# Optimization experiments

Hardware: AMD Instinct MI355X
Metric: run time of the kernel (lower is better)

Reference implementation:

```python
import jax, jax.numpy as jnp
import numpy as np

N, F, H, R, DEG, K = 8192, 64, 128, 3, 32, 32
TEMP = 0.3          # config.edge_temperature
NEG_SLOPE = 0.2     # LeakyReLU slope
EPS_LN = 1e-5
W_THRESH = 1e-6


def setup_inputs() -> dict:
    key = jax.random.key(0)
    ks = jax.random.split(key, 16)
    E = N * DEG
    # each node has DEG outgoing edges so no softmax row is empty (-inf everywhere)
    src = jnp.repeat(jnp.arange(N), DEG)
    tgt = jax.random.randint(ks[0], (E,), 0, N)
    edge_index = jnp.stack([src, tgt]).astype(jnp.int64)
    x = jax.random.normal(ks[1], (N, F), jnp.float32)
    edge_attr = jax.random.normal(ks[2], (E, 3), jnp.float32)
    s = lambda k, sh: jax.random.normal(k, sh, jnp.float32) * 0.05
    D = 2 * F + 3  # edge_input_dim
    params = dict(
        Ws1=s(ks[3], (D, H)), bs1=jnp.zeros(H), ln_g=jnp.ones(H), ln_b=jnp.zeros(H),
        Ws2=s(ks[4], (H, 1)), bs2=jnp.zeros(1),
        Wp=s(ks[5], (D, H)), bp=jnp.zeros(H),
        Wr1=s(ks[6], (F, H)), br1=jnp.zeros(H), Wr2=s(ks[7], (H, R)), br2=jnp.zeros(R),
        Wg1=s(ks[8], (R, H, H // 2)), bg1=jnp.zeros((R, H // 2)),
        Wg2=s(ks[9], (R, H // 2, 1)), bg2=jnp.zeros((R, 1)),
        Wc1=s(ks[10], (F, H)), bc1=jnp.zeros(H), Wc2=s(ks[11], (H, 1)), bc2=jnp.zeros(1),
    )
    return {"x": x, "edge_index": edge_index, "edge_attr": edge_attr, **params}


def reference(x, edge_index, edge_attr,
              Ws1, bs1, ln_g, ln_b, Ws2, bs2, Wp, bp,
              Wr1, br1, Wr2, br2, Wg1, bg1, Wg2, bg2,
              Wc1, bc1, Wc2, bc2):
    src, tgt = edge_index[0], edge_index[1]
    num_nodes = x.shape[0]

    # regime encoder on global mean state
    gs = x.mean(axis=0)
    regime_probs = jax.nn.softmax(jax.nn.relu(gs @ Wr1 + br1) @ Wr2 + br2)  # [R]

    # contagion detector (scalar level)
    contagion_level = jax.nn.sigmoid(jax.nn.relu(x @ Wc1 + bc1) @ Wc2 + bc2).mean()

    # gather -> edge MLP scorer with LayerNorm + LeakyReLU
    edge_input = jnp.concatenate([x[src], x[tgt], edge_attr], axis=-1)  # [E, 2F+3]
    h = edge_input @ Ws1 + bs1
    mu = h.mean(-1, keepdims=True)
    var = h.var(-1, keepdims=True)
    h = (h - mu) * jax.lax.rsqrt(var + EPS_LN) * ln_g + ln_b
    h = jnp.where(h >= 0, h, NEG_SLOPE * h)
    edge_scores_raw = h @ Ws2 + bs2  # [E, 1]

    # regime gating
    edge_hidden = jax.nn.relu(edge_input @ Wp + bp)  # [E, H]
    g1 = jax.nn.relu(jnp.einsum('eh,rhm->erm', edge_hidden, Wg1) + bg1)
    gates = jax.nn.sigmoid(jnp.einsum('erm,rmo->ero', g1, Wg2) + bg2)[..., 0]  # [E, R]
    gate_combined = (gates * regime_probs).sum(-1, keepdims=True)  # [E, 1]

    amp = 1.0 + 0.5 * contagion_level
    edge_scores = (edge_scores_raw * gate_combined * amp)[:, 0]  # [E]

    # scatter into dense NxN, masked softmax per source row, top-k
    M = jnp.full((num_nodes, num_nodes), -jnp.inf, x.dtype).at[src, tgt].set(edge_scores)
    P = jax.nn.softmax(M / TEMP, axis=-1)  # [N, N]
    topk_values, topk_indices = jax.lax.top_k(P, K)  # [N, K]

    # in-device compaction equivalent: weights below threshold zeroed (dropped edges)
    new_edge_weights = jnp.where(topk_values > W_THRESH, topk_values, 0.0)  # [N, K]
    return new_edge_weights, topk_indices
```

## Files before the change

kernel.cpp:

```cpp
#include <hip/hip_runtime.h>
#include <hip/hip_bf16.h>
#include <math.h>

#define NN 8192
#define FF 64
#define HH 128
#define RR 3
#define DEG 32
#define KK 32
#define EE (NN*DEG)
#define DD 131
#define TEMP 0.3f
#define NEG_SLOPE 0.2f
#define EPS_LN 1e-5f
#define W_THRESH 1e-6f

__device__ __forceinline__ float4 ld4(const float* p) { return *(const float4*)p; }


__global__ __launch_bounds__(256) void stats_kernel(
    const float* __restrict__ x, const float* __restrict__ Wc1,
    const float* __restrict__ bc1, const float* __restrict__ Wc2,
    const float* __restrict__ bc2, float* __restrict__ hdr)
{
    __shared__ float xs[64 * 65];
    __shared__ float wl[64 * 128];
    __shared__ float cs[4][64];
    int t = threadIdx.x;
    int n0 = blockIdx.x * 64;

    for (int i = 0; i < 16; i++) {
        int flat = t + i * 256;
        int r = flat >> 6, c = flat & 63;
        xs[r * 65 + c] = x[(n0 + r) * 64 + c];
    }
    for (int i = 0; i < 32; i++) {
        int flat = t + i * 256;
        wl[flat] = Wc1[flat];
    }
    __syncthreads();

    {
        int col = t & 63, g = t >> 6;
        float ps = 0.f;
        for (int r = g * 16; r < g * 16 + 16; r++) ps += xs[r * 65 + col];
        cs[g][col] = ps;
    }
    __syncthreads();
    if (t < 64) {
        float v = cs[0][t] + cs[1][t] + cs[2][t] + cs[3][t];
        atomicAdd(&hdr[8 + t], v);
    }

    int r = t >> 2, q = t & 3;
    float accl = 0.f;
    for (int hh = 0; hh < 32; hh++) {
        int h = hh * 4 + q;
        float s = bc1[h];
        for (int i = 0; i < 64; i++) s += xs[r * 65 + i] * wl[i * 128 + h];
        accl += fmaxf(s, 0.f) * Wc2[h];
    }
    accl += __shfl_xor(accl, 1);
    accl += __shfl_xor(accl, 2);
    if (q == 0) {
        float lvl = 1.f / (1.f + expf(-(accl + bc2[0])));
        atomicAdd(&hdr[0], lvl);
    }
}

__global__ __launch_bounds__(128) void regime_kernel(
    const float* __restrict__ Wr1, const float* __restrict__ br1,
    const float* __restrict__ Wr2, const float* __restrict__ br2,
    float* __restrict__ hdr)
{
    __shared__ float gsl[64];
    __shared__ float t1[128];
    int t = threadIdx.x;
    if (t < 64) gsl[t] = hdr[8 + t] * (1.f / (float)NN);
    __syncthreads();
    float a = br1[t];
    for (int i = 0; i < 64; i++) a += gsl[i] * Wr1[i * 128 + t];
    t1[t] = fmaxf(a, 0.f);
    __syncthreads();
    if (t < 3) {
        float v = br2[t];
        for (int h = 0; h < 128; h++) v += t1[h] * Wr2[h * 3 + t];
        gsl[32 + t] = v;
    }
    __syncthreads();
    if (t == 0) {
        float v0 = gsl[32], v1 = gsl[33], v2 = gsl[34];
        float m = fmaxf(v0, fmaxf(v1, v2));
        float e0 = expf(v0 - m), e1 = expf(v1 - m), e2 = expf(v2 - m);
        float inv = 1.f / (e0 + e1 + e2);
        hdr[1] = e0 * inv; hdr[2] = e1 * inv; hdr[3] = e2 * inv;
        hdr[4] = 1.f + 0.5f * (hdr[0] * (1.f / (float)NN));
    }
}

__global__ __launch_bounds__(256) void partial_kernel(
    const float* __restrict__ x, const float* __restrict__ Ws1,
    const float* __restrict__ Wp, float* __restrict__ PA)
{
    __shared__ float xs[32 * 65];
    __shared__ float wl[64 * 128];
    int t = threadIdx.x;
    int which = blockIdx.x & 1;
    int n0 = (blockIdx.x >> 1) * 32;
    const float* base = which ? Wp : Ws1;

    for (int i = t; i < 2048; i += 256)
        xs[(i >> 6) * 65 + (i & 63)] = x[n0 * 64 + i];
    for (int it = 0; it < 8; it++) {
        int flat = (t + it * 256) * 4;
        *(float4*)&wl[flat] = ld4(&base[flat]);
    }
    __syncthreads();

    int row = t >> 3, colg = t & 7;
    float acc[16];
    #pragma unroll
    for (int j = 0; j < 16; j++) acc[j] = 0.f;
    const float* xr = &xs[row * 65];
    for (int k = 0; k < 64; k++) {
        float a = xr[k];
        const float* wr = &wl[k * 128 + colg * 16];
        #pragma unroll
        for (int jj = 0; jj < 4; jj++) {
            float4 w = ld4(wr + 4 * jj);
            acc[4*jj+0] += a * w.x; acc[4*jj+1] += a * w.y;
            acc[4*jj+2] += a * w.z; acc[4*jj+3] += a * w.w;
        }
    }
    float* outp = PA + (size_t)which * (NN * 128) + (size_t)(n0 + row) * 128 + colg * 16;
    #pragma unroll
    for (int j = 0; j < 16; j++) outp[j] = acc[j];
}

#define EIB_STRIDE 76
#define EHT_STRIDE 68
__global__ __launch_bounds__(256) void edge_score_kernel(
    const int* __restrict__ tgt_idx, const float* __restrict__ edge_attr,
    const float* __restrict__ x,
    const float* __restrict__ Ws1, const float* __restrict__ bs1,
    const float* __restrict__ ln_g, const float* __restrict__ ln_b,
    const float* __restrict__ Ws2, const float* __restrict__ bs2,
    const float* __restrict__ Wp, const float* __restrict__ bp,
    const float* __restrict__ Wg1, const float* __restrict__ bg1,
    const float* __restrict__ Wg2, const float* __restrict__ bg2,
    const float* __restrict__ PA1, const float* __restrict__ PA2,
    const float* __restrict__ hdr, float* __restrict__ scores)
{
    __shared__ float pool[13184];
    float* EIB   = pool;
    float* WPan  = pool + 4864;
    float* ehT   = pool;
    float* WgG   = pool + 8704;
    float* rawS  = pool + 13056;
    float* gateC = pool + 13120;

    int t = threadIdx.x;
    int e0 = blockIdx.x * 64;

    {
        int r = t >> 2, q = t & 3;
        int ge = e0 + r;
        int tg = tgt_idx[ge];
        for (int ii = q; ii < EIB_STRIDE; ii += 4) {
            float v;
            if (ii < 64) v = x[tg * 64 + ii];
            else if (ii < 67) v = edge_attr[ge * 3 + (ii - 64)];
            else v = 0.f;
            EIB[r * EIB_STRIDE + ii] = v;
        }
    }

    int tcol = t & 7, trow = t >> 3;
    const float* EIr0 = &EIB[(2 * trow) * EIB_STRIDE];
    const float* EIr1 = EIr0 + EIB_STRIDE;
    int src0 = (e0 + 2 * trow) >> 5;
    int src1 = (e0 + 2 * trow + 1) >> 5;

    float accs0[16], accs1[16], accp0[16], accp1[16];

    {
        const float* p1a = &PA1[(size_t)src0 * 128 + tcol * 4];
        const float* p1b = &PA1[(size_t)src1 * 128 + tcol * 4];
        const float* p2a = &PA2[(size_t)src0 * 128 + tcol * 4];
        const float* p2b = &PA2[(size_t)src1 * 128 + tcol * 4];
        #pragma unroll
        for (int jj = 0; jj < 4; jj++) {
            float4 v;
            v = ld4(p1a + jj * 32);
            accs0[4*jj+0]=v.x; accs0[4*jj+1]=v.y; accs0[4*jj+2]=v.z; accs0[4*jj+3]=v.w;
            v = ld4(p1b + jj * 32);
            accs1[4*jj+0]=v.x; accs1[4*jj+1]=v.y; accs1[4*jj+2]=v.z; accs1[4*jj+3]=v.w;
            v = ld4(p2a + jj * 32);
            accp0[4*jj+0]=v.x; accp0[4*jj+1]=v.y; accp0[4*jj+2]=v.z; accp0[4*jj+3]=v.w;
            v = ld4(p2b + jj * 32);
            accp1[4*jj+0]=v.x; accp1[4*jj+1]=v.y; accp1[4*jj+2]=v.z; accp1[4*jj+3]=v.w;
        }
    }

    for (int p = 0; p < 3; p++) {
        __syncthreads();
        #pragma unroll
        for (int i = 0; i < 6; i++) {
            int fid = i * 256 + t;
            int mat = (fid >= 768) ? 1 : 0;
            int loc = fid - mat * 768;
            int pr = loc >> 5;
            int pc = (loc & 31) * 4;
            int wrow = 64 + p * 24 + pr;
            const float* Wsrc = mat ? Wp : Ws1;
            float4 w = (wrow < 131) ? ld4(&Wsrc[wrow * 128 + pc])
                                    : make_float4(0.f, 0.f, 0.f, 0.f);
            *(float4*)&WPan[mat * 3072 + pr * 128 + pc] = w;
        }
        __syncthreads();
        for (int kk = 0; kk < 24; kk++) {
            int k = p * 24 + kk;
            float a0 = EIr0[k];
            float a1 = EIr1[k];
            const float* ws = &WPan[kk * 128 + tcol * 4];
            const float* wq = &WPan[3072 + kk * 128 + tcol * 4];
            #pragma unroll
            for (int jj = 0; jj < 4; jj++) {
                float4 w1 = ld4(ws + jj * 32);
                accs0[jj*4+0] += a0 * w1.x; accs0[jj*4+1] += a0 * w1.y;
                accs0[jj*4+2] += a0 * w1.z; accs0[jj*4+3] += a0 * w1.w;
                accs1[jj*4+0] += a1 * w1.x; accs1[jj*4+1] += a1 * w1.y;
                accs1[jj*4+2] += a1 * w1.z; accs1[jj*4+3] += a1 * w1.w;
                float4 w2 = ld4(wq + jj * 32);
                accp0[jj*4+0] += a0 * w2.x; accp0[jj*4+1] += a0 * w2.y;
                accp0[jj*4+2] += a0 * w2.z; accp0[jj*4+3] += a0 * w2.w;
                accp1[jj*4+0] += a1 * w2.x; accp1[jj*4+1] += a1 * w2.y;
                accp1[jj*4+2] += a1 * w2.z; accp1[jj*4+3] += a1 * w2.w;
            }
        }
    }

    {
        float s0 = 0.f, ss0 = 0.f, s1 = 0.f, ss1 = 0.f;
        #pragma unroll
        for (int j = 0; j < 16; j++) {
            int col = tcol * 4 + (j >> 2) * 32 + (j & 3);
            float b = bs1[col];
            accs0[j] += b; accs1[j] += b;
            s0 += accs0[j]; ss0 += accs0[j] * accs0[j];
            s1 += accs1[j]; ss1 += accs1[j] * accs1[j];
        }
        #pragma unroll
        for (int m = 1; m < 8; m <<= 1) {
            s0 += __shfl_xor(s0, m);  ss0 += __shfl_xor(ss0, m);
            s1 += __shfl_xor(s1, m);  ss1 += __shfl_xor(ss1, m);
        }
        float mu0 = s0 * (1.f / 128.f), mu1 = s1 * (1.f / 128.f);
        float var0 = ss0 * (1.f / 128.f) - mu0 * mu0;
        float var1 = ss1 * (1.f / 128.f) - mu1 * mu1;
        float inv0 = 1.f / sqrtf(var0 + EPS_LN);
        float inv1 = 1.f / sqrtf(var1 + EPS_LN);
        float d0 = 0.f, d1 = 0.f;
        #pragma unroll
        for (int j = 0; j < 16; j++) {
            int col = tcol * 4 + (j >> 2) * 32 + (j & 3);
            float g = ln_g[col], bb = ln_b[col], w2 = Ws2[col];
            float y0 = (accs0[j] - mu0) * inv0 * g + bb;
            float y1 = (accs1[j] - mu1) * inv1 * g + bb;
            y0 = (y0 >= 0.f) ? y0 : NEG_SLOPE * y0;
            y1 = (y1 >= 0.f) ? y1 : NEG_SLOPE * y1;
            d0 += y0 * w2; d1 += y1 * w2;
        }
        #pragma unroll
        for (int m = 1; m < 8; m <<= 1) {
            d0 += __shfl_xor(d0, m); d1 += __shfl_xor(d1, m);
        }
        if (tcol == 0) {
            rawS[2 * trow]     = d0 + bs2[0];
            rawS[2 * trow + 1] = d1 + bs2[0];
        }
    }

    __syncthreads();
    #pragma unroll
    for (int j = 0; j < 16; j++) {
        int col = tcol * 4 + (j >> 2) * 32 + (j & 3);
        float b = bp[col];
        ehT[col * EHT_STRIDE + 2 * trow]     = fmaxf(accp0[j] + b, 0.f);
        ehT[col * EHT_STRIDE + 2 * trow + 1] = fmaxf(accp1[j] + b, 0.f);
    }

    {
        int gtr = t >> 4, gtc = t & 15;
        int grow = t >> 2, gq = t & 3;
        float rp0 = hdr[1], rp1 = hdr[2], rp2 = hdr[3];
        float gc = 0.f;
        for (int rr = 0; rr < 3; rr++) {
            float acc[16];
            #pragma unroll
            for (int j = 0; j < 16; j++) acc[j] = 0.f;
            for (int p = 0; p < 2; p++) {
                __syncthreads();
                #pragma unroll
                for (int i = 0; i < 4; i++) {
                    int fid = i * 256 + t;
                    int pr = fid >> 4;
                    int pc = (fid & 15) * 4;
                    *(float4*)&WgG[pr * 64 + pc] =
                        ld4(&Wg1[(size_t)(rr * 128 + p * 64 + pr) * 64 + pc]);
                }
                __syncthreads();
                for (int kk = 0; kk < 64; kk++) {
                    float4 av = ld4(&ehT[(p * 64 + kk) * EHT_STRIDE + 4 * gtr]);
                    float4 bv = ld4(&WgG[kk * 64 + 4 * gtc]);
                    acc[0]  += av.x * bv.x; acc[1]  += av.x * bv.y; acc[2]  += av.x * bv.z; acc[3]  += av.x * bv.w;
                    acc[4]  += av.y * bv.x; acc[5]  += av.y * bv.y; acc[6]  += av.y * bv.z; acc[7]  += av.y * bv.w;
                    acc[8]  += av.z * bv.x; acc[9]  += av.z * bv.y; acc[10] += av.z * bv.z; acc[11] += av.z * bv.w;
                    acc[12] += av.w * bv.x; acc[13] += av.w * bv.y; acc[14] += av.w * bv.z; acc[15] += av.w * bv.w;
                }
            }
            __syncthreads();
            #pragma unroll
            for (int j = 0; j < 4; j++) {
                float b = bg1[rr * 64 + 4 * gtc + j];
                float4 g;
                g.x = fmaxf(acc[0  + j] + b, 0.f);
                g.y = fmaxf(acc[4  + j] + b, 0.f);
                g.z = fmaxf(acc[8  + j] + b, 0.f);
                g.w = fmaxf(acc[12 + j] + b, 0.f);
                *(float4*)&WgG[(4 * gtc + j) * EHT_STRIDE + 4 * gtr] = g;
            }
            __syncthreads();
            float pacc = 0.f;
            #pragma unroll
            for (int j = 0; j < 16; j++) {
                int m = gq * 4 + (j >> 2) * 16 + (j & 3);
                pacc += WgG[m * EHT_STRIDE + grow] * Wg2[rr * 64 + m];
            }
            pacc += __shfl_xor(pacc, 1);
            pacc += __shfl_xor(pacc, 2);
            float gate = 1.f / (1.f + expf(-(pacc + bg2[rr])));
            float rpr = (rr == 0) ? rp0 : ((rr == 1) ? rp1 : rp2);
            gc += gate * rpr;
        }
        if (gq == 0) gateC[grow] = gc;
    }
    __syncthreads();

    if (t < 64) scores[e0 + t] = rawS[t] * gateC[t] * hdr[4];
}

__global__ __launch_bounds__(64) void finalize_kernel(
    const int* __restrict__ tgt_idx, const float* __restrict__ scores,
    float* __restrict__ out_w, float* __restrict__ out_i)
{
    __shared__ int   tl[32];
    __shared__ float pl[32];
    int j = threadIdx.x;
    int row = blockIdx.x;
    bool lane_active = (j < 32);
    int   tg = 0;
    float s  = -INFINITY;
    if (lane_active) {
        tg = tgt_idx[row * 32 + j];
        s  = scores[row * 32 + j];
        tl[j] = tg;
    }
    __syncthreads();

    bool alive = false;
    if (lane_active) {
        alive = true;
        for (int j2 = j + 1; j2 < 32; j2++)
            if (tl[j2] == tg) { alive = false; break; }
    }
    float z = (lane_active && alive) ? s * (1.f / TEMP) : -INFINITY;
    float m = z;
    #pragma unroll
    for (int mm = 1; mm < 64; mm <<= 1) m = fmaxf(m, __shfl_xor(m, mm));
    float p = (lane_active && alive) ? expf(z - m) : 0.f;
    float sum = p;
    #pragma unroll
    for (int mm = 1; mm < 64; mm <<= 1) sum += __shfl_xor(sum, mm);
    p = p / sum;
    if (lane_active) pl[j] = alive ? p : -1.f;
    __syncthreads();

    int rank = 0, dcount = 0;
    for (int j2 = 0; j2 < 32; j2++) {
        float pj = pl[j2];
        if (pj >= 0.f) {
            dcount++;
            if (lane_active && alive) {
                if (pj > p || (pj == p && tl[j2] < tg)) rank++;
            }
        }
    }
    if (lane_active && alive) {
        out_w[row * 32 + rank] = (p > W_THRESH) ? p : 0.f;
        out_i[row * 32 + rank] = (float)tg;
    }
    if (j == 0) {
        int c = 0;
        for (int slot = dcount; slot < 32; slot++) {
            for (;;) {
                bool found = false;
                for (int q = 0; q < 32; q++) if (tl[q] == c) { found = true; break; }
                if (!found) break;
                c++;
            }
            out_w[row * 32 + slot] = 0.f;
            out_i[row * 32 + slot] = (float)c;
            c++;
        }
    }
}

extern "C" void kernel_launch(void* const* d_in, const int* in_sizes, int n_in,
                              void* d_out, int out_size, void* d_ws, size_t ws_size,
                              hipStream_t stream)
{
    const float* x          = (const float*)d_in[0];
    const int*   edge_index = (const int*)  d_in[1];
    const float* edge_attr  = (const float*)d_in[2];
    const float* Ws1 = (const float*)d_in[3];
    const float* bs1 = (const float*)d_in[4];
    const float* ln_g = (const float*)d_in[5];
    const float* ln_b = (const float*)d_in[6];
    const float* Ws2 = (const float*)d_in[7];
    const float* bs2 = (const float*)d_in[8];
    const float* Wp  = (const float*)d_in[9];
    const float* bp  = (const float*)d_in[10];
    const float* Wr1 = (const float*)d_in[11];
    const float* br1 = (const float*)d_in[12];
    const float* Wr2 = (const float*)d_in[13];
    const float* br2 = (const float*)d_in[14];
    const float* Wg1 = (const float*)d_in[15];
    const float* bg1 = (const float*)d_in[16];
    const float* Wg2 = (const float*)d_in[17];
    const float* bg2 = (const float*)d_in[18];
    const float* Wc1 = (const float*)d_in[19];
    const float* bc1 = (const float*)d_in[20];
    const float* Wc2 = (const float*)d_in[21];
    const float* bc2 = (const float*)d_in[22];

    float* hdr    = (float*)d_ws;
    float* scores = hdr + 128;
    float* tabs   = scores + EE;
    const int* tgt = edge_index + EE;

    hipMemsetAsync(d_ws, 0, 512, stream);
    stats_kernel<<<128, 256, 0, stream>>>(x, Wc1, bc1, Wc2, bc2, hdr);
    regime_kernel<<<1, 128, 0, stream>>>(Wr1, br1, Wr2, br2, hdr);
    partial_kernel<<<(NN / 32) * 2, 256, 0, stream>>>(x, Ws1, Wp, tabs);
    edge_score_kernel<<<EE / 64, 256, 0, stream>>>(
        tgt, edge_attr, x, Ws1, bs1, ln_g, ln_b, Ws2, bs2, Wp, bp,
        Wg1, bg1, Wg2, bg2, tabs, tabs + (size_t)NN * 128, hdr, scores);
    finalize_kernel<<<NN, 64, 0, stream>>>(
        tgt, scores, (float*)d_out, (float*)d_out + NN * KK);
}
```

Baseline: 517.8 us.

## Process 128 edges per block with transposed edge inputs and fused regime GEMMs

Doubles edges per block to 128 and stores edge inputs transposed so each thread computes a 4-edge by 16-column tile, reusing each weight load across four edges. The Ws1 and Wp projections now run as two separate passes sharing one accumulator array. The three regime gate GEMMs are fused into one k-loop over two 64-edge halves, reusing each ehT load across three weight panels. The aim is fewer shared-memory loads per FMA and fewer weight panel reloads per edge, at the cost of higher register pressure (48 gate accumulators plus edge accumulators) that may cut occupancy, and half as many blocks.

```diff
diff --git a/kernel.cpp b/kernel.cpp
--- a/kernel.cpp
+++ b/kernel.cpp
@@ -137,8 +137,6 @@
     for (int j = 0; j < 16; j++) outp[j] = acc[j];
 }
 
-#define EIB_STRIDE 76
-#define EHT_STRIDE 68
 __global__ __launch_bounds__(256) void edge_score_kernel(
     const int* __restrict__ tgt_idx, const float* __restrict__ edge_attr,
     const float* __restrict__ x,
@@ -151,203 +149,272 @@
     const float* __restrict__ PA1, const float* __restrict__ PA2,
     const float* __restrict__ hdr, float* __restrict__ scores)
 {
-    __shared__ float pool[13184];
-    float* EIB   = pool;
-    float* WPan  = pool + 4864;
+    __shared__ float pool[12864];
+    float* EIBT  = pool;
+    float* WPan  = pool + 9504;
     float* ehT   = pool;
-    float* WgG   = pool + 8704;
-    float* rawS  = pool + 13056;
-    float* gateC = pool + 13120;
+    float* WgPan = pool + 8704;
+    float* Gbuf  = pool;
+    float* rawS  = pool + 12608;
+    float* gateC = pool + 12736;
 
     int t = threadIdx.x;
-    int e0 = blockIdx.x * 64;
+    int e0 = blockIdx.x * 128;
 
     {
-        int r = t >> 2, q = t & 3;
-        int ge = e0 + r;
-        int tg = tgt_idx[ge];
-        for (int ii = q; ii < EIB_STRIDE; ii += 4) {
-            float v;
-            if (ii < 64) v = x[tg * 64 + ii];
-            else if (ii < 67) v = edge_attr[ge * 3 + (ii - 64)];
-            else v = 0.f;
-            EIB[r * EIB_STRIDE + ii] = v;
-        }
-    }
-
-    int tcol = t & 7, trow = t >> 3;
-    const float* EIr0 = &EIB[(2 * trow) * EIB_STRIDE];
-    const float* EIr1 = EIr0 + EIB_STRIDE;
-    int src0 = (e0 + 2 * trow) >> 5;
-    int src1 = (e0 + 2 * trow + 1) >> 5;
-
-    float accs0[16], accs1[16], accp0[16], accp1[16];
+        int e = t >> 1, q = t & 1;
+        int tg = tgt_idx[e0 + e];
+        #pragma unroll
+        for (int i = 0; i < 8; i++) {
+            float4 v = ld4(&x[tg * 64 + q * 32 + 4 * i]);
+            int k = q * 32 + 4 * i;
+            EIBT[(k + 0) * 132 + e] = v.x;
+            EIBT[(k + 1) * 132 + e] = v.y;
+            EIBT[(k + 2) * 132 + e] = v.z;
+            EIBT[(k + 3) * 132 + e] = v.w;
+        }
+        #pragma unroll
+        for (int i = 0; i < 4; i++) {
+            int flat = t + i * 256;
+            int k = 64 + (flat >> 7);
+            int e2 = flat & 127;
+            float v = (k < 67) ? edge_attr[(size_t)(e0 + e2) * 3 + (k - 64)] : 0.f;
+            EIBT[k * 132 + e2] = v;
+        }
+    }
+
+    int tcol = t & 7, eg = t >> 3;
+    int src = (e0 + 4 * eg) >> 5;
+
+    float acc[4][16];
 
     {
-        const float* p1a = &PA1[(size_t)src0 * 128 + tcol * 4];
-        const float* p1b = &PA1[(size_t)src1 * 128 + tcol * 4];
-        const float* p2a = &PA2[(size_t)src0 * 128 + tcol * 4];
-        const float* p2b = &PA2[(size_t)src1 * 128 + tcol * 4];
+        const float* pp = &PA1[(size_t)src * 128 + tcol * 4];
         #pragma unroll
         for (int jj = 0; jj < 4; jj++) {
-            float4 v;
-            v = ld4(p1a + jj * 32);
-            accs0[4*jj+0]=v.x; accs0[4*jj+1]=v.y; accs0[4*jj+2]=v.z; accs0[4*jj+3]=v.w;
-            v = ld4(p1b + jj * 32);
-            accs1[4*jj+0]=v.x; accs1[4*jj+1]=v.y; accs1[4*jj+2]=v.z; accs1[4*jj+3]=v.w;
-            v = ld4(p2a + jj * 32);
-            accp0[4*jj+0]=v.x; accp0[4*jj+1]=v.y; accp0[4*jj+2]=v.z; accp0[4*jj+3]=v.w;
-            v = ld4(p2b + jj * 32);
-            accp1[4*jj+0]=v.x; accp1[4*jj+1]=v.y; accp1[4*jj+2]=v.z; accp1[4*jj+3]=v.w;
-        }
-    }
-
+            float4 v = ld4(pp + jj * 32);
+            #pragma unroll
+            for (int i = 0; i < 4; i++) {
+                acc[i][4*jj+0] = v.x; acc[i][4*jj+1] = v.y;
+                acc[i][4*jj+2] = v.z; acc[i][4*jj+3] = v.w;
+            }
+        }
+    }
     for (int p = 0; p < 3; p++) {
         __syncthreads();
         #pragma unroll
-        for (int i = 0; i < 6; i++) {
+        for (int i = 0; i < 3; i++) {
             int fid = i * 256 + t;
-            int mat = (fid >= 768) ? 1 : 0;
-            int loc = fid - mat * 768;
-            int pr = loc >> 5;
-            int pc = (loc & 31) * 4;
+            int pr = fid >> 5;
+            int pc = (fid & 31) * 4;
             int wrow = 64 + p * 24 + pr;
-            const float* Wsrc = mat ? Wp : Ws1;
-            float4 w = (wrow < 131) ? ld4(&Wsrc[wrow * 128 + pc])
+            float4 w = (wrow < 131) ? ld4(&Ws1[wrow * 128 + pc])
                                     : make_float4(0.f, 0.f, 0.f, 0.f);
-            *(float4*)&WPan[mat * 3072 + pr * 128 + pc] = w;
+            *(float4*)&WPan[pr * 128 + pc] = w;
         }
         __syncthreads();
         for (int kk = 0; kk < 24; kk++) {
             int k = p * 24 + kk;
-            float a0 = EIr0[k];
-            float a1 = EIr1[k];
-            const float* ws = &WPan[kk * 128 + tcol * 4];
-            const float* wq = &WPan[3072 + kk * 128 + tcol * 4];
+            float4 a = ld4(&EIBT[k * 132 + 4 * eg]);
+            const float* wr = &WPan[kk * 128 + tcol * 4];
             #pragma unroll
             for (int jj = 0; jj < 4; jj++) {
-                float4 w1 = ld4(ws + jj * 32);
-                accs0[jj*4+0] += a0 * w1.x; accs0[jj*4+1] += a0 * w1.y;
-                accs0[jj*4+2] += a0 * w1.z; accs0[jj*4+3] += a0 * w1.w;
-                accs1[jj*4+0] += a1 * w1.x; accs1[jj*4+1] += a1 * w1.y;
-                accs1[jj*4+2] += a1 * w1.z; accs1[jj*4+3] += a1 * w1.w;
-                float4 w2 = ld4(wq + jj * 32);
-                accp0[jj*4+0] += a0 * w2.x; accp0[jj*4+1] += a0 * w2.y;
-                accp0[jj*4+2] += a0 * w2.z; accp0[jj*4+3] += a0 * w2.w;
-                accp1[jj*4+0] += a1 * w2.x; accp1[jj*4+1] += a1 * w2.y;
-                accp1[jj*4+2] += a1 * w2.z; accp1[jj*4+3] += a1 * w2.w;
+                float4 w = ld4(wr + jj * 32);
+                acc[0][jj*4+0] += a.x * w.x; acc[0][jj*4+1] += a.x * w.y;
+                acc[0][jj*4+2] += a.x * w.z; acc[0][jj*4+3] += a.x * w.w;
+                acc[1][jj*4+0] += a.y * w.x; acc[1][jj*4+1] += a.y * w.y;
+                acc[1][jj*4+2] += a.y * w.z; acc[1][jj*4+3] += a.y * w.w;
+                acc[2][jj*4+0] += a.z * w.x; acc[2][jj*4+1] += a.z * w.y;
+                acc[2][jj*4+2] += a.z * w.z; acc[2][jj*4+3] += a.z * w.w;
+                acc[3][jj*4+0] += a.w * w.x; acc[3][jj*4+1] += a.w * w.y;
+                acc[3][jj*4+2] += a.w * w.z; acc[3][jj*4+3] += a.w * w.w;
             }
         }
     }
 
     {
-        float s0 = 0.f, ss0 = 0.f, s1 = 0.f, ss1 = 0.f;
+        float s[4], ss[4];
+        #pragma unroll
+        for (int i = 0; i < 4; i++) { s[i] = 0.f; ss[i] = 0.f; }
         #pragma unroll
         for (int j = 0; j < 16; j++) {
             int col = tcol * 4 + (j >> 2) * 32 + (j & 3);
             float b = bs1[col];
-            accs0[j] += b; accs1[j] += b;
-            s0 += accs0[j]; ss0 += accs0[j] * accs0[j];
-            s1 += accs1[j]; ss1 += accs1[j] * accs1[j];
+            #pragma unroll
+            for (int i = 0; i < 4; i++) {
+                acc[i][j] += b;
+                s[i] += acc[i][j]; ss[i] += acc[i][j] * acc[i][j];
+            }
         }
         #pragma unroll
         for (int m = 1; m < 8; m <<= 1) {
-            s0 += __shfl_xor(s0, m);  ss0 += __shfl_xor(ss0, m);
-            s1 += __shfl_xor(s1, m);  ss1 += __shfl_xor(ss1, m);
-        }
-        float mu0 = s0 * (1.f / 128.f), mu1 = s1 * (1.f / 128.f);
-        float var0 = ss0 * (1.f / 128.f) - mu0 * mu0;
-        float var1 = ss1 * (1.f / 128.f) - mu1 * mu1;
-        float inv0 = 1.f / sqrtf(var0 + EPS_LN);
-        float inv1 = 1.f / sqrtf(var1 + EPS_LN);
-        float d0 = 0.f, d1 = 0.f;
+            #pragma unroll
+            for (int i = 0; i < 4; i++) {
+                s[i] += __shfl_xor(s[i], m);
+                ss[i] += __shfl_xor(ss[i], m);
+            }
+        }
+        float mu[4], inv[4], d[4];
+        #pragma unroll
+        for (int i = 0; i < 4; i++) {
+            mu[i] = s[i] * (1.f / 128.f);
+            float var = ss[i] * (1.f / 128.f) - mu[i] * mu[i];
+            inv[i] = 1.f / sqrtf(var + EPS_LN);
+            d[i] = 0.f;
+        }
         #pragma unroll
         for (int j = 0; j < 16; j++) {
             int col = tcol * 4 + (j >> 2) * 32 + (j & 3);
             float g = ln_g[col], bb = ln_b[col], w2 = Ws2[col];
-            float y0 = (accs0[j] - mu0) * inv0 * g + bb;
-            float y1 = (accs1[j] - mu1) * inv1 * g + bb;
-            y0 = (y0 >= 0.f) ? y0 : NEG_SLOPE * y0;
-            y1 = (y1 >= 0.f) ? y1 : NEG_SLOPE * y1;
-            d0 += y0 * w2; d1 += y1 * w2;
+            #pragma unroll
+            for (int i = 0; i < 4; i++) {
+                float y = (acc[i][j] - mu[i]) * inv[i] * g + bb;
+                y = (y >= 0.f) ? y : NEG_SLOPE * y;
+                d[i] += y * w2;
+            }
         }
         #pragma unroll
         for (int m = 1; m < 8; m <<= 1) {
-            d0 += __shfl_xor(d0, m); d1 += __shfl_xor(d1, m);
+            #pragma unroll
+            for (int i = 0; i < 4; i++) d[i] += __shfl_xor(d[i], m);
         }
         if (tcol == 0) {
-            rawS[2 * trow]     = d0 + bs2[0];
-            rawS[2 * trow + 1] = d1 + bs2[0];
-        }
-    }
-
-    __syncthreads();
-    #pragma unroll
-    for (int j = 0; j < 16; j++) {
-        int col = tcol * 4 + (j >> 2) * 32 + (j & 3);
-        float b = bp[col];
-        ehT[col * EHT_STRIDE + 2 * trow]     = fmaxf(accp0[j] + b, 0.f);
-        ehT[col * EHT_STRIDE + 2 * trow + 1] = fmaxf(accp1[j] + b, 0.f);
+            #pragma unroll
+            for (int i = 0; i < 4; i++) rawS[4 * eg + i] = d[i] + bs2[0];
+        }
     }
 
     {
-        int gtr = t >> 4, gtc = t & 15;
-        int grow = t >> 2, gq = t & 3;
-        float rp0 = hdr[1], rp1 = hdr[2], rp2 = hdr[3];
+        const float* pp = &PA2[(size_t)src * 128 + tcol * 4];
+        #pragma unroll
+        for (int jj = 0; jj < 4; jj++) {
+            float4 v = ld4(pp + jj * 32);
+            #pragma unroll
+            for (int i = 0; i < 4; i++) {
+                acc[i][4*jj+0] = v.x; acc[i][4*jj+1] = v.y;
+                acc[i][4*jj+2] = v.z; acc[i][4*jj+3] = v.w;
+            }
+        }
+    }
+    for (int p = 0; p < 3; p++) {
+        __syncthreads();
+        #pragma unroll
+        for (int i = 0; i < 3; i++) {
+            int fid = i * 256 + t;
+            int pr = fid >> 5;
+            int pc = (fid & 31) * 4;
+            int wrow = 64 + p * 24 + pr;
+            float4 w = (wrow < 131) ? ld4(&Wp[wrow * 128 + pc])
+                                    : make_float4(0.f, 0.f, 0.f, 0.f);
+            *(float4*)&WPan[pr * 128 + pc] = w;
+        }
+        __syncthreads();
+        for (int kk = 0; kk < 24; kk++) {
+            int k = p * 24 + kk;
+            float4 a = ld4(&EIBT[k * 132 + 4 * eg]);
+            const float* wr = &WPan[kk * 128 + tcol * 4];
+            #pragma unroll
+            for (int jj = 0; jj < 4; jj++) {
+                float4 w = ld4(wr + jj * 32);
+                acc[0][jj*4+0] += a.x * w.x; acc[0][jj*4+1] += a.x * w.y;
+                acc[0][jj*4+2] += a.x * w.z; acc[0][jj*4+3] += a.x * w.w;
+                acc[1][jj*4+0] += a.y * w.x; acc[1][jj*4+1] += a.y * w.y;
+                acc[1][jj*4+2] += a.y * w.z; acc[1][jj*4+3] += a.y * w.w;
+                acc[2][jj*4+0] += a.z * w.x; acc[2][jj*4+1] += a.z * w.y;
+                acc[2][jj*4+2] += a.z * w.z; acc[2][jj*4+3] += a.z * w.w;
+                acc[3][jj*4+0] += a.w * w.x; acc[3][jj*4+1] += a.w * w.y;
+                acc[3][jj*4+2] += a.w * w.z; acc[3][jj*4+3] += a.w * w.w;
+            }
+        }
+    }
+    __syncthreads();
+
+    int gtr = t >> 4, gtc = t & 15;
+    int grow = t >> 2, gq = t & 3;
+
+    for (int h = 0; h < 2; h++) {
+        if (h) __syncthreads();
+        if ((eg >> 4) == h) {
+            int e4 = (4 * eg) & 63;
+            #pragma unroll
+            for (int j = 0; j < 16; j++) {
+                int col = tcol * 4 + (j >> 2) * 32 + (j & 3);
+                float b = bp[col];
+                float4 g;
+                g.x = fmaxf(acc[0][j] + b, 0.f);
+                g.y = fmaxf(acc[1][j] + b, 0.f);
+                g.z = fmaxf(acc[2][j] + b, 0.f);
+                g.w = fmaxf(acc[3][j] + b, 0.f);
+                *(float4*)&ehT[col * 68 + e4] = g;
+            }
+        }
+
+        float gacc[3][16];
+        #pragma unroll
+        for (int r = 0; r < 3; r++)
+            #pragma unroll
+            for (int j = 0; j < 16; j++) gacc[r][j] = 0.f;
+
+        for (int p = 0; p < 8; p++) {
+            __syncthreads();
+            {
+                int pr = t >> 4;
+                int pc = (t & 15) * 4;
+                #pragma unroll
+                for (int r = 0; r < 3; r++)
+                    *(float4*)&WgPan[r * 1024 + pr * 64 + pc] =
+                        ld4(&Wg1[(size_t)(r * 128 + p * 16 + pr) * 64 + pc]);
+            }
+            __syncthreads();
+            for (int kk = 0; kk < 16; kk++) {
+                float4 av = ld4(&ehT[(p * 16 + kk) * 68 + 4 * gtr]);
+                #pragma unroll
+                for (int r = 0; r < 3; r++) {
+                    float4 bv = ld4(&WgPan[r * 1024 + kk * 64 + 4 * gtc]);
+                    gacc[r][0]  += av.x * bv.x; gacc[r][1]  += av.x * bv.y;
+                    gacc[r][2]  += av.x * bv.z; gacc[r][3]  += av.x * bv.w;
+                    gacc[r][4]  += av.y * bv.x; gacc[r][5]  += av.y * bv.y;
+                    gacc[r][6]  += av.y * bv.z; gacc[r][7]  += av.y * bv.w;
+                    gacc[r][8]  += av.z * bv.x; gacc[r][9]  += av.z * bv.y;
+                    gacc[r][10] += av.z * bv.z; gacc[r][11] += av.z * bv.w;
+                    gacc[r][12] += av.w * bv.x; gacc[r][13] += av.w * bv.y;
+                    gacc[r][14] += av.w * bv.z; gacc[r][15] += av.w * bv.w;
+                }
+            }
+        }
+        __syncthreads();
+        #pragma unroll
+        for (int r = 0; r < 3; r++) {
+            #pragma unroll
+            for (int j = 0; j < 4; j++) {
+                float b = bg1[r * 64 + 4 * gtc + j];
+                float4 g;
+                g.x = fmaxf(gacc[r][0  + j] + b, 0.f);
+                g.y = fmaxf(gacc[r][4  + j] + b, 0.f);
+                g.z = fmaxf(gacc[r][8  + j] + b, 0.f);
+                g.w = fmaxf(gacc[r][12 + j] + b, 0.f);
+                *(float4*)&Gbuf[r * 4160 + (4 * gtc + j) * 65 + 4 * gtr] = g;
+            }
+        }
+        __syncthreads();
         float gc = 0.f;
-        for (int rr = 0; rr < 3; rr++) {
-            float acc[16];
-            #pragma unroll
-            for (int j = 0; j < 16; j++) acc[j] = 0.f;
-            for (int p = 0; p < 2; p++) {
-                __syncthreads();
-                #pragma unroll
-                for (int i = 0; i < 4; i++) {
-                    int fid = i * 256 + t;
-                    int pr = fid >> 4;
-                    int pc = (fid & 15) * 4;
-                    *(float4*)&WgG[pr * 64 + pc] =
-                        ld4(&Wg1[(size_t)(rr * 128 + p * 64 + pr) * 64 + pc]);
-                }
-                __syncthreads();
-                for (int kk = 0; kk < 64; kk++) {
-                    float4 av = ld4(&ehT[(p * 64 + kk) * EHT_STRIDE + 4 * gtr]);
-                    float4 bv = ld4(&WgG[kk * 64 + 4 * gtc]);
-                    acc[0]  += av.x * bv.x; acc[1]  += av.x * bv.y; acc[2]  += av.x * bv.z; acc[3]  += av.x * bv.w;
-                    acc[4]  += av.y * bv.x; acc[5]  += av.y * bv.y; acc[6]  += av.y * bv.z; acc[7]  += av.y * bv.w;
-                    acc[8]  += av.z * bv.x; acc[9]  += av.z * bv.y; acc[10] += av.z * bv.z; acc[11] += av.z * bv.w;
-                    acc[12] += av.w * bv.x; acc[13] += av.w * bv.y; acc[14] += av.w * bv.z; acc[15] += av.w * bv.w;
-                }
-            }
-            __syncthreads();
-            #pragma unroll
-            for (int j = 0; j < 4; j++) {
-                float b = bg1[rr * 64 + 4 * gtc + j];
-                float4 g;
-                g.x = fmaxf(acc[0  + j] + b, 0.f);
-                g.y = fmaxf(acc[4  + j] + b, 0.f);
-                g.z = fmaxf(acc[8  + j] + b, 0.f);
-                g.w = fmaxf(acc[12 + j] + b, 0.f);
-                *(float4*)&WgG[(4 * gtc + j) * EHT_STRIDE + 4 * gtr] = g;
-            }
-            __syncthreads();
+        for (int r = 0; r < 3; r++) {
             float pacc = 0.f;
             #pragma unroll
             for (int j = 0; j < 16; j++) {
                 int m = gq * 4 + (j >> 2) * 16 + (j & 3);
-                pacc += WgG[m * EHT_STRIDE + grow] * Wg2[rr * 64 + m];
+                pacc += Gbuf[r * 4160 + m * 65 + grow] * Wg2[r * 64 + m];
             }
             pacc += __shfl_xor(pacc, 1);
             pacc += __shfl_xor(pacc, 2);
-            float gate = 1.f / (1.f + expf(-(pacc + bg2[rr])));
-            float rpr = (rr == 0) ? rp0 : ((rr == 1) ? rp1 : rp2);
-            gc += gate * rpr;
-        }
-        if (gq == 0) gateC[grow] = gc;
-    }
-    __syncthreads();
-
-    if (t < 64) scores[e0 + t] = rawS[t] * gateC[t] * hdr[4];
+            float gate = 1.f / (1.f + expf(-(pacc + bg2[r])));
+            gc += gate * hdr[1 + r];
+        }
+        if (gq == 0) gateC[h * 64 + grow] = gc;
+    }
+    __syncthreads();
+
+    if (t < 128) scores[e0 + t] = rawS[t] * gateC[t] * hdr[4];
 }
 
 __global__ __launch_bounds__(64) void finalize_kernel(
@@ -453,7 +520,7 @@
     stats_kernel<<<128, 256, 0, stream>>>(x, Wc1, bc1, Wc2, bc2, hdr);
     regime_kernel<<<1, 128, 0, stream>>>(Wr1, br1, Wr2, br2, hdr);
     partial_kernel<<<(NN / 32) * 2, 256, 0, stream>>>(x, Ws1, Wp, tabs);
-    edge_score_kernel<<<EE / 64, 256, 0, stream>>>(
+    edge_score_kernel<<<EE / 128, 256, 0, stream>>>(
         tgt, edge_attr, x, Ws1, bs1, ln_g, ln_b, Ws2, bs2, Wp, bp,
         Wg1, bg1, Wg2, bg2, tabs, tabs + (size_t)NN * 128, hdr, scores);
     finalize_kernel<<<NN, 64, 0, stream>>>(
```

Result: slower. 614.5 us (+18.7%).

## Split fused edge kernel into GEMM/LayerNorm and gating kernels via workspace

Applied to the files above, without the earlier changes.

Splits the fused edge scoring kernel into two kernels. The first does the edge-input GEMMs, LayerNorm and the raw score, then writes the ReLU hidden activations (E x 128 floats) to global workspace. The second computes all three regime gates in one pass, reading Wg1 directly from global memory instead of staging it in shared memory. Smaller shared-memory footprints and launch_bounds(256,5) aim at higher occupancy, and a per-edge-pair source-row load is deduplicated. The trade is a large extra global write and read of the hidden tensor (about 128MB), with a fallback to the fused kernel when the workspace is too small.

```diff
diff --git a/kernel.cpp b/kernel.cpp
--- a/kernel.cpp
+++ b/kernel.cpp
@@ -137,9 +137,229 @@
     for (int j = 0; j < 16; j++) outp[j] = acc[j];
 }
 
-#define EIB_STRIDE 76
+#define EIB_S 72
+__global__ __launch_bounds__(256, 5) void gemm_kernel(
+    const int* __restrict__ tgt_idx, const float* __restrict__ edge_attr,
+    const float* __restrict__ x,
+    const float* __restrict__ Ws1, const float* __restrict__ bs1,
+    const float* __restrict__ ln_g, const float* __restrict__ ln_b,
+    const float* __restrict__ Ws2, const float* __restrict__ bs2,
+    const float* __restrict__ Wp, const float* __restrict__ bp,
+    const float* __restrict__ PA1, const float* __restrict__ PA2,
+    float* __restrict__ rawSG, float* __restrict__ ehG)
+{
+    __shared__ float pool[7680];
+    float* EIB  = pool;
+    float* WPan = pool + 4608;
+    float* ehTh = pool;
+
+    int t = threadIdx.x;
+    int e0 = blockIdx.x * 64;
+
+    {
+        int r = t >> 2, q = t & 3;
+        int ge = e0 + r;
+        int tg = tgt_idx[ge];
+        for (int ii = q; ii < EIB_S; ii += 4) {
+            float v;
+            if (ii < 64) v = x[tg * 64 + ii];
+            else if (ii < 67) v = edge_attr[(size_t)ge * 3 + (ii - 64)];
+            else v = 0.f;
+            EIB[r * EIB_S + ii] = v;
+        }
+    }
+
+    int tcol = t & 7, trow = t >> 3;
+    const float* EIr0 = &EIB[(2 * trow) * EIB_S];
+    const float* EIr1 = EIr0 + EIB_S;
+    int src = (e0 + 2 * trow) >> 5;
+
+    float accs0[16], accs1[16], accp0[16], accp1[16];
+
+    {
+        const float* p1 = &PA1[(size_t)src * 128 + tcol * 4];
+        const float* p2 = &PA2[(size_t)src * 128 + tcol * 4];
+        #pragma unroll
+        for (int jj = 0; jj < 4; jj++) {
+            float4 v;
+            v = ld4(p1 + jj * 32);
+            accs0[4*jj+0]=v.x; accs0[4*jj+1]=v.y; accs0[4*jj+2]=v.z; accs0[4*jj+3]=v.w;
+            accs1[4*jj+0]=v.x; accs1[4*jj+1]=v.y; accs1[4*jj+2]=v.z; accs1[4*jj+3]=v.w;
+            v = ld4(p2 + jj * 32);
+            accp0[4*jj+0]=v.x; accp0[4*jj+1]=v.y; accp0[4*jj+2]=v.z; accp0[4*jj+3]=v.w;
+            accp1[4*jj+0]=v.x; accp1[4*jj+1]=v.y; accp1[4*jj+2]=v.z; accp1[4*jj+3]=v.w;
+        }
+    }
+
+    for (int p = 0; p < 6; p++) {
+        __syncthreads();
+        #pragma unroll
+        for (int i = 0; i < 3; i++) {
+            int fid = i * 256 + t;
+            int mat = (fid >= 384) ? 1 : 0;
+            int loc = fid - mat * 384;
+            int pr = loc >> 5;
+            int pc = (loc & 31) * 4;
+            int wrow = 64 + p * 12 + pr;
+            const float* Wsrc = mat ? Wp : Ws1;
+            float4 w = (wrow < 131) ? ld4(&Wsrc[wrow * 128 + pc])
+                                    : make_float4(0.f, 0.f, 0.f, 0.f);
+            *(float4*)&WPan[mat * 1536 + pr * 128 + pc] = w;
+        }
+        __syncthreads();
+        for (int kk = 0; kk < 12; kk++) {
+            int k = p * 12 + kk;
+            float a0 = EIr0[k];
+            float a1 = EIr1[k];
+            const float* ws = &WPan[kk * 128 + tcol * 4];
+            const float* wq = &WPan[1536 + kk * 128 + tcol * 4];
+            #pragma unroll
+            for (int jj = 0; jj < 4; jj++) {
+                float4 w1 = ld4(ws + jj * 32);
+                accs0[jj*4+0] += a0 * w1.x; accs0[jj*4+1] += a0 * w1.y;
+                accs0[jj*4+2] += a0 * w1.z; accs0[jj*4+3] += a0 * w1.w;
+                accs1[jj*4+0] += a1 * w1.x; accs1[jj*4+1] += a1 * w1.y;
+                accs1[jj*4+2] += a1 * w1.z; accs1[jj*4+3] += a1 * w1.w;
+                float4 w2 = ld4(wq + jj * 32);
+                accp0[jj*4+0] += a0 * w2.x; accp0[jj*4+1] += a0 * w2.y;
+                accp0[jj*4+2] += a0 * w2.z; accp0[jj*4+3] += a0 * w2.w;
+                accp1[jj*4+0] += a1 * w2.x; accp1[jj*4+1] += a1 * w2.y;
+                accp1[jj*4+2] += a1 * w2.z; accp1[jj*4+3] += a1 * w2.w;
+            }
+        }
+    }
+
+    {
+        float s0 = 0.f, ss0 = 0.f, s1 = 0.f, ss1 = 0.f;
+        #pragma unroll
+        for (int j = 0; j < 16; j++) {
+            int col = tcol * 4 + (j >> 2) * 32 + (j & 3);
+            float b = bs1[col];
+            accs0[j] += b; accs1[j] += b;
+            s0 += accs0[j]; ss0 += accs0[j] * accs0[j];
+            s1 += accs1[j]; ss1 += accs1[j] * accs1[j];
+        }
+        #pragma unroll
+        for (int m = 1; m < 8; m <<= 1) {
+            s0 += __shfl_xor(s0, m);  ss0 += __shfl_xor(ss0, m);
+            s1 += __shfl_xor(s1, m);  ss1 += __shfl_xor(ss1, m);
+        }
+        float mu0 = s0 * (1.f / 128.f), mu1 = s1 * (1.f / 128.f);
+        float var0 = ss0 * (1.f / 128.f) - mu0 * mu0;
+        float var1 = ss1 * (1.f / 128.f) - mu1 * mu1;
+        float inv0 = 1.f / sqrtf(var0 + EPS_LN);
+        float inv1 = 1.f / sqrtf(var1 + EPS_LN);
+        float d0 = 0.f, d1 = 0.f;
+        #pragma unroll
+        for (int j = 0; j < 16; j++) {
+            int col = tcol * 4 + (j >> 2) * 32 + (j & 3);
+            float g = ln_g[col], bb = ln_b[col], w2 = Ws2[col];
+            float y0 = (accs0[j] - mu0) * inv0 * g + bb;
+            float y1 = (accs1[j] - mu1) * inv1 * g + bb;
+            y0 = (y0 >= 0.f) ? y0 : NEG_SLOPE * y0;
+            y1 = (y1 >= 0.f) ? y1 : NEG_SLOPE * y1;
+            d0 += y0 * w2; d1 += y1 * w2;
+        }
+        #pragma unroll
+        for (int m = 1; m < 8; m <<= 1) {
+            d0 += __shfl_xor(d0, m); d1 += __shfl_xor(d1, m);
+        }
+        if (tcol == 0) {
+            rawSG[e0 + 2 * trow]     = d0 + bs2[0];
+            rawSG[e0 + 2 * trow + 1] = d1 + bs2[0];
+        }
+    }
+
+    for (int hf = 0; hf < 2; hf++) {
+        __syncthreads();
+        #pragma unroll
+        for (int j = 0; j < 8; j++) {
+            int jj = hf * 8 + j;
+            int col = tcol * 4 + (jj >> 2) * 32 + (jj & 3);
+            int lc = col - hf * 64;
+            float b = bp[col];
+            ehTh[lc * 68 + 2 * trow]     = fmaxf(accp0[jj] + b, 0.f);
+            ehTh[lc * 68 + 2 * trow + 1] = fmaxf(accp1[jj] + b, 0.f);
+        }
+        __syncthreads();
+        #pragma unroll
+        for (int i = 0; i < 4; i++) {
+            int idx = i * 256 + t;
+            int lc = idx >> 4;
+            int m4 = (idx & 15) * 4;
+            float4 v = ld4(&ehTh[lc * 68 + m4]);
+            *(float4*)&ehG[(size_t)blockIdx.x * 8192 + (size_t)(hf * 64 + lc) * 64 + m4] = v;
+        }
+    }
+}
+
+__global__ __launch_bounds__(256, 5) void gating_kernel(
+    const float* __restrict__ ehG, const float* __restrict__ rawSG,
+    const float* __restrict__ Wg1, const float* __restrict__ bg1,
+    const float* __restrict__ Wg2, const float* __restrict__ bg2,
+    const float* __restrict__ hdr, float* __restrict__ scores)
+{
+    __shared__ float Gbuf[64 * 68];
+    int t = threadIdx.x;
+    int e0 = blockIdx.x * 64;
+    int gtr = t >> 4, gtc = t & 15;
+    int grow = t >> 2, gq = t & 3;
+
+    const float* A = ehG + (size_t)blockIdx.x * 8192;
+
+    float gacc[3][16];
+    #pragma unroll
+    for (int r = 0; r < 3; r++)
+        #pragma unroll
+        for (int j = 0; j < 16; j++) gacc[r][j] = 0.f;
+
+    #pragma unroll 2
+    for (int k = 0; k < 128; k++) {
+        float4 av = ld4(&A[k * 64 + 4 * gtr]);
+        #pragma unroll
+        for (int r = 0; r < 3; r++) {
+            float4 bv = ld4(&Wg1[(size_t)(r * 128 + k) * 64 + 4 * gtc]);
+            gacc[r][0]  += av.x * bv.x; gacc[r][1]  += av.x * bv.y;
+            gacc[r][2]  += av.x * bv.z; gacc[r][3]  += av.x * bv.w;
+            gacc[r][4]  += av.y * bv.x; gacc[r][5]  += av.y * bv.y;
+            gacc[r][6]  += av.y * bv.z; gacc[r][7]  += av.y * bv.w;
+            gacc[r][8]  += av.z * bv.x; gacc[r][9]  += av.z * bv.y;
+            gacc[r][10] += av.z * bv.z; gacc[r][11] += av.z * bv.w;
+            gacc[r][12] += av.w * bv.x; gacc[r][13] += av.w * bv.y;
+            gacc[r][14] += av.w * bv.z; gacc[r][15] += av.w * bv.w;
+        }
+    }
+
+    float gc = 0.f;
+    for (int r = 0; r < 3; r++) {
+        if (r) __syncthreads();
+        #pragma unroll
+        for (int j = 0; j < 4; j++) {
+            float b = bg1[r * 64 + 4 * gtc + j];
+            float4 g;
+            g.x = fmaxf(gacc[r][0  + j] + b, 0.f);
+            g.y = fmaxf(gacc[r][4  + j] + b, 0.f);
+            g.z = fmaxf(gacc[r][8  + j] + b, 0.f);
+            g.w = fmaxf(gacc[r][12 + j] + b, 0.f);
+            *(float4*)&Gbuf[(4 * gtc + j) * 68 + 4 * gtr] = g;
+        }
+        __syncthreads();
+        float pacc = 0.f;
+        #pragma unroll
+        for (int j = 0; j < 16; j++) {
+            int m = gq * 4 + (j >> 2) * 16 + (j & 3);
+            pacc += Gbuf[m * 68 + grow] * Wg2[r * 64 + m];
+        }
+        pacc += __shfl_xor(pacc, 1);
+        pacc += __shfl_xor(pacc, 2);
+        float gate = 1.f / (1.f + expf(-(pacc + bg2[r])));
+        gc += gate * hdr[1 + r];
+    }
+    if (gq == 0) scores[e0 + grow] = rawSG[e0 + grow] * gc * hdr[4];
+}
+
 #define EHT_STRIDE 68
-__global__ __launch_bounds__(256) void edge_score_kernel(
+__global__ __launch_bounds__(256) void edge_fused_kernel(
     const int* __restrict__ tgt_idx, const float* __restrict__ edge_attr,
     const float* __restrict__ x,
     const float* __restrict__ Ws1, const float* __restrict__ bs1,
@@ -166,38 +386,32 @@
         int r = t >> 2, q = t & 3;
         int ge = e0 + r;
         int tg = tgt_idx[ge];
-        for (int ii = q; ii < EIB_STRIDE; ii += 4) {
+        for (int ii = q; ii < 76; ii += 4) {
             float v;
             if (ii < 64) v = x[tg * 64 + ii];
-            else if (ii < 67) v = edge_attr[ge * 3 + (ii - 64)];
+            else if (ii < 67) v = edge_attr[(size_t)ge * 3 + (ii - 64)];
             else v = 0.f;
-            EIB[r * EIB_STRIDE + ii] = v;
+            EIB[r * 76 + ii] = v;
         }
     }
 
     int tcol = t & 7, trow = t >> 3;
-    const float* EIr0 = &EIB[(2 * trow) * EIB_STRIDE];
-    const float* EIr1 = EIr0 + EIB_STRIDE;
-    int src0 = (e0 + 2 * trow) >> 5;
-    int src1 = (e0 + 2 * trow + 1) >> 5;
+    const float* EIr0 = &EIB[(2 * trow) * 76];
+    const float* EIr1 = EIr0 + 76;
+    int src = (e0 + 2 * trow) >> 5;
 
     float accs0[16], accs1[16], accp0[16], accp1[16];
-
-    {
-        const float* p1a = &PA1[(size_t)src0 * 128 + tcol * 4];
-        const float* p1b = &PA1[(size_t)src1 * 128 + tcol * 4];
-        const float* p2a = &PA2[(size_t)src0 * 128 + tcol * 4];
-        const float* p2b = &PA2[(size_t)src1 * 128 + tcol * 4];
+    {
+        const float* p1 = &PA1[(size_t)src * 128 + tcol * 4];
+        const float* p2 = &PA2[(size_t)src * 128 + tcol * 4];
         #pragma unroll
         for (int jj = 0; jj < 4; jj++) {
             float4 v;
-            v = ld4(p1a + jj * 32);
+            v = ld4(p1 + jj * 32);
             accs0[4*jj+0]=v.x; accs0[4*jj+1]=v.y; accs0[4*jj+2]=v.z; accs0[4*jj+3]=v.w;
-            v = ld4(p1b + jj * 32);
             accs1[4*jj+0]=v.x; accs1[4*jj+1]=v.y; accs1[4*jj+2]=v.z; accs1[4*jj+3]=v.w;
-            v = ld4(p2a + jj * 32);
+            v = ld4(p2 + jj * 32);
             accp0[4*jj+0]=v.x; accp0[4*jj+1]=v.y; accp0[4*jj+2]=v.z; accp0[4*jj+3]=v.w;
-            v = ld4(p2b + jj * 32);
             accp1[4*jj+0]=v.x; accp1[4*jj+1]=v.y; accp1[4*jj+2]=v.z; accp1[4*jj+3]=v.w;
         }
     }
@@ -293,7 +507,6 @@
     {
         int gtr = t >> 4, gtc = t & 15;
         int grow = t >> 2, gq = t & 3;
-        float rp0 = hdr[1], rp1 = hdr[2], rp2 = hdr[3];
         float gc = 0.f;
         for (int rr = 0; rr < 3; rr++) {
             float acc[16];
@@ -340,8 +553,7 @@
             pacc += __shfl_xor(pacc, 1);
             pacc += __shfl_xor(pacc, 2);
             float gate = 1.f / (1.f + expf(-(pacc + bg2[rr])));
-            float rpr = (rr == 0) ? rp0 : ((rr == 1) ? rp1 : rp2);
-            gc += gate * rpr;
+            gc += gate * hdr[1 + rr];
         }
         if (gq == 0) gateC[grow] = gc;
     }
@@ -447,15 +659,29 @@
     float* hdr    = (float*)d_ws;
     float* scores = hdr + 128;
     float* tabs   = scores + EE;
+    float* rawSG  = tabs + 2 * (size_t)NN * 128;
+    float* ehG    = rawSG + EE;
     const int* tgt = edge_index + EE;
+
+    size_t need_split = (size_t)(128 + EE + 2 * (size_t)NN * 128 + EE) * 4
+                      + (size_t)EE * 128 * 4;
 
     hipMemsetAsync(d_ws, 0, 512, stream);
     stats_kernel<<<128, 256, 0, stream>>>(x, Wc1, bc1, Wc2, bc2, hdr);
     regime_kernel<<<1, 128, 0, stream>>>(Wr1, br1, Wr2, br2, hdr);
     partial_kernel<<<(NN / 32) * 2, 256, 0, stream>>>(x, Ws1, Wp, tabs);
-    edge_score_kernel<<<EE / 64, 256, 0, stream>>>(
-        tgt, edge_attr, x, Ws1, bs1, ln_g, ln_b, Ws2, bs2, Wp, bp,
-        Wg1, bg1, Wg2, bg2, tabs, tabs + (size_t)NN * 128, hdr, scores);
+
+    if (ws_size >= need_split) {
+        gemm_kernel<<<EE / 64, 256, 0, stream>>>(
+            tgt, edge_attr, x, Ws1, bs1, ln_g, ln_b, Ws2, bs2, Wp, bp,
+            tabs, tabs + (size_t)NN * 128, rawSG, ehG);
+        gating_kernel<<<EE / 64, 256, 0, stream>>>(
+            ehG, rawSG, Wg1, bg1, Wg2, bg2, hdr, scores);
+    } else {
+        edge_fused_kernel<<<EE / 64, 256, 0, stream>>>(
+            tgt, edge_attr, x, Ws1, bs1, ln_g, ln_b, Ws2, bs2, Wp, bp,
+            Wg1, bg1, Wg2, bg2, tabs, tabs + (size_t)NN * 128, hdr, scores);
+    }
     finalize_kernel<<<NN, 64, 0, stream>>>(
         tgt, scores, (float*)d_out, (float*)d_out + NN * KK);
 }
```

Result: slower. 607.7 us (+17.4%).
